# Kernel tuning notes

Hardware: AMD Instinct MI355X
Metric: run time of the kernel (lower is better)

Reference implementation:

```python
import jax, jax.numpy as jnp
import numpy as np
from jax.scipy.fft import dct

B, C, H, W = 64, 3, 512, 512


def dct2(x):
    # 2D DCT-II with ortho norm, matching scipy.fft.dct applied on axis=-1 then axis=-2
    x = dct(x, type=2, norm='ortho', axis=-1)
    x = dct(x, type=2, norm='ortho', axis=-2)
    return x


def setup_inputs() -> dict:
    key = jax.random.key(0)
    k1, k2, k3, k4 = jax.random.split(key, 4)
    return {
        'x': jax.random.normal(k1, (B, C, H, W), dtype=jnp.float32),
        'attention': jax.random.uniform(k2, (H, W), dtype=jnp.float32),
        'row_weights': jax.random.uniform(k3, (H,), dtype=jnp.float32),
        'col_weights': jax.random.uniform(k4, (W,), dtype=jnp.float32),
    }


def reference(x, attention, row_weights, col_weights):
    xd = dct2(x)                       # [B, C, H, W]
    gray = xd.mean(axis=1)             # [B, H, W] (channel mean)
    weighted = gray * attention        # [B, H, W]
    row_sum = weighted.mean(axis=2)    # [B, H] mean over W
    col_sum = weighted.mean(axis=1)    # [B, W] mean over H
    row_out = (row_sum * row_weights).mean(axis=1)  # [B]
    col_out = (col_sum * col_weights).mean(axis=1)  # [B]
    return jax.nn.sigmoid(jnp.stack([col_out, row_out], axis=1))  # [B, 2]
```

## Files before the change

kernel.cpp:

```cpp
#include <hip/hip_runtime.h>
#include <math.h>

#define NN 512
#define MM (NN * NN)
#define HW (NN * NN)
#define CH 3

__device__ __forceinline__ float dct_s(int k) {
    return (k == 0) ? 0.04419417382415922f : 0.0625f;
}

__global__ void __launch_bounds__(256) k_stageA(
    const float* __restrict__ att, const float* __restrict__ rw,
    const float* __restrict__ cw, float* __restrict__ Tr, float* __restrict__ Tc)
{
    __shared__ float sD[2048];
    __shared__ float sRw[512];
    __shared__ float sAcc[256 * 9];
    const int tid = threadIdx.x;
    const int bx  = blockIdx.x;
    const int h0  = (bx >> 3) * 4;
    const int wp0 = (bx & 7) * 64;
    const int kc  = tid >> 6;
    const int wl  = tid & 63;
    const int wp  = wp0 + wl;
    const int hp0 = kc * 128;

    #pragma unroll
    for (int e = 0; e < 8; ++e) {
        int idx = tid * 8 + e;
        int hp = idx >> 2, i = idx & 3;
        int m = ((2 * (h0 + i) + 1) * hp) & 2047;
        sD[idx] = dct_s(hp) * cospif((float)m * (1.0f / 1024.0f));
    }
    sRw[tid] = rw[tid];
    sRw[256 + tid] = rw[256 + tid];
    __syncthreads();

    float ar0=0.f,ar1=0.f,ar2=0.f,ar3=0.f, as0=0.f,as1=0.f,as2=0.f,as3=0.f;
    #pragma unroll 4
    for (int t = 0; t < 128; ++t) {
        int hp = hp0 + t;
        float a = att[hp * NN + wp];
        float r = sRw[hp];
        float4 d = *reinterpret_cast<const float4*>(&sD[hp * 4]);
        float ra = r * a;
        ar0 += d.x * ra; as0 += d.x * a;
        ar1 += d.y * ra; as1 += d.y * a;
        ar2 += d.z * ra; as2 += d.z * a;
        ar3 += d.w * ra; as3 += d.w * a;
    }
    float* sa = &sAcc[tid * 9];
    sa[0]=ar0; sa[1]=ar1; sa[2]=ar2; sa[3]=ar3;
    sa[4]=as0; sa[5]=as1; sa[6]=as2; sa[7]=as3;
    __syncthreads();
    if (tid < 64) {
        float v[8];
        #pragma unroll
        for (int j = 0; j < 8; ++j)
            v[j] = sAcc[(0*64 + tid)*9 + j] + sAcc[(1*64 + tid)*9 + j]
                 + sAcc[(2*64 + tid)*9 + j] + sAcc[(3*64 + tid)*9 + j];
        float c = cw[wp0 + tid];
        #pragma unroll
        for (int i = 0; i < 4; ++i) {
            Tr[(h0 + i) * NN + wp0 + tid] = v[i];
            Tc[(h0 + i) * NN + wp0 + tid] = v[4 + i] * c;
        }
    }
}

__global__ void __launch_bounds__(256) k_stageB(
    const float* __restrict__ Tr, const float* __restrict__ Tc,
    float* __restrict__ Gr, float* __restrict__ Gc)
{
    __shared__ float sT[512 * 8];
    __shared__ float sAcc[256 * 9];
    const int tid = threadIdx.x;
    const int bx  = blockIdx.x;
    const int h0  = (bx >> 3) * 4;
    const int w0  = (bx & 7) * 64;
    const int kc  = tid >> 6;
    const int wl  = tid & 63;
    const int w   = w0 + wl;
    const int wp0 = kc * 128;

    #pragma unroll
    for (int i = 0; i < 4; ++i) {
        sT[tid * 8 + i]             = Tr[(h0 + i) * NN + tid];
        sT[tid * 8 + 4 + i]         = Tc[(h0 + i) * NN + tid];
        sT[(tid + 256) * 8 + i]     = Tr[(h0 + i) * NN + tid + 256];
        sT[(tid + 256) * 8 + 4 + i] = Tc[(h0 + i) * NN + tid + 256];
    }
    __syncthreads();

    float gr0=0.f,gr1=0.f,gr2=0.f,gr3=0.f, gc0=0.f,gc1=0.f,gc2=0.f,gc3=0.f;
    const int w2 = 2 * w + 1;
    int m = (w2 * wp0) & 2047;
    #pragma unroll 4
    for (int t = 0; t < 128; ++t) {
        int wp = wp0 + t;
        float s = (wp == 0) ? 0.04419417382415922f : 0.0625f;
        float d = s * cospif((float)m * (1.0f / 1024.0f));
        m = (m + w2) & 2047;
        float4 ta = *reinterpret_cast<const float4*>(&sT[wp * 8]);
        float4 tb = *reinterpret_cast<const float4*>(&sT[wp * 8 + 4]);
        gr0 += ta.x * d; gr1 += ta.y * d; gr2 += ta.z * d; gr3 += ta.w * d;
        gc0 += tb.x * d; gc1 += tb.y * d; gc2 += tb.z * d; gc3 += tb.w * d;
    }
    float* sa = &sAcc[tid * 9];
    sa[0]=gr0; sa[1]=gr1; sa[2]=gr2; sa[3]=gr3;
    sa[4]=gc0; sa[5]=gc1; sa[6]=gc2; sa[7]=gc3;
    __syncthreads();
    if (tid < 64) {
        float v[8];
        #pragma unroll
        for (int j = 0; j < 8; ++j)
            v[j] = sAcc[(0*64 + tid)*9 + j] + sAcc[(1*64 + tid)*9 + j]
                 + sAcc[(2*64 + tid)*9 + j] + sAcc[(3*64 + tid)*9 + j];
        #pragma unroll
        for (int i = 0; i < 4; ++i) {
            Gr[(h0 + i) * NN + w0 + tid] = v[i];
            Gc[(h0 + i) * NN + w0 + tid] = v[4 + i];
        }
    }
}

__global__ void __launch_bounds__(256) k_reduce(
    const float* __restrict__ x, const float* __restrict__ Gr,
    const float* __restrict__ Gc, float* __restrict__ partials)
{
    const int b = blockIdx.y, ck = blockIdx.x, t = threadIdx.x;
    const float* xb = x + (size_t)b * (CH * HW);
    const int hw0 = ck * (HW / 32);
    float accr = 0.f, accc = 0.f;
    #pragma unroll 4
    for (int j = 0; j < 8; ++j) {
        int hw = hw0 + j * 1024 + t * 4;
        float4 gr = *(const float4*)(Gr + hw);
        float4 gc = *(const float4*)(Gc + hw);
        float4 x0 = *(const float4*)(xb + hw);
        float4 x1 = *(const float4*)(xb + HW + hw);
        float4 x2 = *(const float4*)(xb + 2 * HW + hw);
        float sxx = x0.x + x1.x + x2.x;
        float sxy = x0.y + x1.y + x2.y;
        float sxz = x0.z + x1.z + x2.z;
        float sxw = x0.w + x1.w + x2.w;
        accr += gr.x * sxx + gr.y * sxy + gr.z * sxz + gr.w * sxw;
        accc += gc.x * sxx + gc.y * sxy + gc.z * sxz + gc.w * sxw;
    }
    for (int off = 32; off > 0; off >>= 1) {
        accr += __shfl_down(accr, off);
        accc += __shfl_down(accc, off);
    }
    __shared__ float sr[4], sc[4];
    int wid = t >> 6;
    if ((t & 63) == 0) { sr[wid] = accr; sc[wid] = accc; }
    __syncthreads();
    if (t == 0) {
        partials[(b * 32 + ck) * 2 + 0] = sr[0] + sr[1] + sr[2] + sr[3];
        partials[(b * 32 + ck) * 2 + 1] = sc[0] + sc[1] + sc[2] + sc[3];
    }
}

__global__ void k_final(const float* __restrict__ partials, float* __restrict__ out) {
    int b = threadIdx.x;
    float r = 0.f, c = 0.f;
    for (int i = 0; i < 32; ++i) {
        r += partials[(b * 32 + i) * 2 + 0];
        c += partials[(b * 32 + i) * 2 + 1];
    }
    const float inv = 1.0f / (float)(CH * HW);
    r *= inv; c *= inv;
    out[b * 2 + 0] = 1.0f / (1.0f + expf(-c));
    out[b * 2 + 1] = 1.0f / (1.0f + expf(-r));
}

extern "C" void kernel_launch(void* const* d_in, const int* in_sizes, int n_in,
                              void* d_out, int out_size, void* d_ws, size_t ws_size,
                              hipStream_t stream) {
    const float* x   = (const float*)d_in[0];
    const float* att = (const float*)d_in[1];
    const float* rw  = (const float*)d_in[2];
    const float* cw  = (const float*)d_in[3];
    float* out = (float*)d_out;

    float* ws = (float*)d_ws;
    float* Tr = ws;
    float* Tc = ws + 1 * MM;
    float* Gr = ws + 2 * MM;
    float* Gc = ws + 3 * MM;
    float* partials = ws + 4 * MM;

    k_stageA<<<1024, 256, 0, stream>>>(att, rw, cw, Tr, Tc);
    k_stageB<<<1024, 256, 0, stream>>>(Tr, Tc, Gr, Gc);
    dim3 g(32, 64);
    k_reduce<<<g, 256, 0, stream>>>(x, Gr, Gc, partials);
    k_final<<<1, 64, 0, stream>>>(partials, out);
}
```

Before: 84.62 us.

## Fuse final reduction into reduce kernel via atomic counter, process two batches per block

Merges the separate final-sum kernel into the reduce kernel using a global atomic counter, so the last block to finish computes the sigmoid outputs. Each reduce block now handles two batches, which halves the grid and reuses each Gr/Gc load across both batches. The change removes one kernel launch and cuts Gr/Gc traffic, at the cost of an atomic, thread fences, and fewer blocks in flight for the memory-bound read of x.

```diff
diff --git a/kernel.cpp b/kernel.cpp
--- a/kernel.cpp
+++ b/kernel.cpp
@@ -12,13 +12,15 @@
 
 __global__ void __launch_bounds__(256) k_stageA(
     const float* __restrict__ att, const float* __restrict__ rw,
-    const float* __restrict__ cw, float* __restrict__ Tr, float* __restrict__ Tc)
+    const float* __restrict__ cw, float* __restrict__ Tr, float* __restrict__ Tc,
+    unsigned int* __restrict__ counter)
 {
     __shared__ float sD[2048];
     __shared__ float sRw[512];
     __shared__ float sAcc[256 * 9];
     const int tid = threadIdx.x;
     const int bx  = blockIdx.x;
+    if (bx == 0 && tid == 0) *counter = 0u;
     const int h0  = (bx >> 3) * 4;
     const int wp0 = (bx & 7) * 64;
     const int kc  = tid >> 6;
@@ -125,54 +127,83 @@
     }
 }
 
-__global__ void __launch_bounds__(256) k_reduce(
+__global__ void __launch_bounds__(256) k_reduce_final(
     const float* __restrict__ x, const float* __restrict__ Gr,
-    const float* __restrict__ Gc, float* __restrict__ partials)
+    const float* __restrict__ Gc, float* __restrict__ partials,
+    unsigned int* __restrict__ counter, float* __restrict__ out)
 {
-    const int b = blockIdx.y, ck = blockIdx.x, t = threadIdx.x;
-    const float* xb = x + (size_t)b * (CH * HW);
+    const int ck = blockIdx.x;
+    const int b1 = blockIdx.y;
+    const int b2 = b1 + 32;
+    const int t  = threadIdx.x;
+    const float* xb1 = x + (size_t)b1 * (CH * HW);
+    const float* xb2 = x + (size_t)b2 * (CH * HW);
     const int hw0 = ck * (HW / 32);
-    float accr = 0.f, accc = 0.f;
-    #pragma unroll 4
+
+    float ar1 = 0.f, ac1 = 0.f, ar2 = 0.f, ac2 = 0.f;
+    #pragma unroll 2
     for (int j = 0; j < 8; ++j) {
         int hw = hw0 + j * 1024 + t * 4;
         float4 gr = *(const float4*)(Gr + hw);
         float4 gc = *(const float4*)(Gc + hw);
-        float4 x0 = *(const float4*)(xb + hw);
-        float4 x1 = *(const float4*)(xb + HW + hw);
-        float4 x2 = *(const float4*)(xb + 2 * HW + hw);
-        float sxx = x0.x + x1.x + x2.x;
-        float sxy = x0.y + x1.y + x2.y;
-        float sxz = x0.z + x1.z + x2.z;
-        float sxw = x0.w + x1.w + x2.w;
-        accr += gr.x * sxx + gr.y * sxy + gr.z * sxz + gr.w * sxw;
-        accc += gc.x * sxx + gc.y * sxy + gc.z * sxz + gc.w * sxw;
+        float4 p0 = *(const float4*)(xb1 + hw);
+        float4 p1 = *(const float4*)(xb1 + HW + hw);
+        float4 p2 = *(const float4*)(xb1 + 2 * HW + hw);
+        float4 q0 = *(const float4*)(xb2 + hw);
+        float4 q1 = *(const float4*)(xb2 + HW + hw);
+        float4 q2 = *(const float4*)(xb2 + 2 * HW + hw);
+        float s1x = p0.x + p1.x + p2.x, s1y = p0.y + p1.y + p2.y;
+        float s1z = p0.z + p1.z + p2.z, s1w = p0.w + p1.w + p2.w;
+        float s2x = q0.x + q1.x + q2.x, s2y = q0.y + q1.y + q2.y;
+        float s2z = q0.z + q1.z + q2.z, s2w = q0.w + q1.w + q2.w;
+        ar1 += gr.x * s1x + gr.y * s1y + gr.z * s1z + gr.w * s1w;
+        ac1 += gc.x * s1x + gc.y * s1y + gc.z * s1z + gc.w * s1w;
+        ar2 += gr.x * s2x + gr.y * s2y + gr.z * s2z + gr.w * s2w;
+        ac2 += gc.x * s2x + gc.y * s2y + gc.z * s2z + gc.w * s2w;
     }
     for (int off = 32; off > 0; off >>= 1) {
-        accr += __shfl_down(accr, off);
-        accc += __shfl_down(accc, off);
-    }
-    __shared__ float sr[4], sc[4];
+        ar1 += __shfl_down(ar1, off);
+        ac1 += __shfl_down(ac1, off);
+        ar2 += __shfl_down(ar2, off);
+        ac2 += __shfl_down(ac2, off);
+    }
+    __shared__ float sm[4][4];
+    __shared__ bool sdone;
     int wid = t >> 6;
-    if ((t & 63) == 0) { sr[wid] = accr; sc[wid] = accc; }
+    if ((t & 63) == 0) {
+        sm[wid][0] = ar1; sm[wid][1] = ac1; sm[wid][2] = ar2; sm[wid][3] = ac2;
+    }
     __syncthreads();
     if (t == 0) {
-        partials[(b * 32 + ck) * 2 + 0] = sr[0] + sr[1] + sr[2] + sr[3];
-        partials[(b * 32 + ck) * 2 + 1] = sc[0] + sc[1] + sc[2] + sc[3];
-    }
-}
-
-__global__ void k_final(const float* __restrict__ partials, float* __restrict__ out) {
-    int b = threadIdx.x;
-    float r = 0.f, c = 0.f;
-    for (int i = 0; i < 32; ++i) {
-        r += partials[(b * 32 + i) * 2 + 0];
-        c += partials[(b * 32 + i) * 2 + 1];
-    }
-    const float inv = 1.0f / (float)(CH * HW);
-    r *= inv; c *= inv;
-    out[b * 2 + 0] = 1.0f / (1.0f + expf(-c));
-    out[b * 2 + 1] = 1.0f / (1.0f + expf(-r));
+        float r1 = sm[0][0] + sm[1][0] + sm[2][0] + sm[3][0];
+        float c1 = sm[0][1] + sm[1][1] + sm[2][1] + sm[3][1];
+        float r2 = sm[0][2] + sm[1][2] + sm[2][2] + sm[3][2];
+        float c2 = sm[0][3] + sm[1][3] + sm[2][3] + sm[3][3];
+        partials[(b1 * 32 + ck) * 2 + 0] = r1;
+        partials[(b1 * 32 + ck) * 2 + 1] = c1;
+        partials[(b2 * 32 + ck) * 2 + 0] = r2;
+        partials[(b2 * 32 + ck) * 2 + 1] = c2;
+        __threadfence();
+        unsigned int old = atomicAdd(counter, 1u);
+        sdone = (old == 32u * 32u - 1u);
+    }
+    __syncthreads();
+    if (sdone) {
+        __threadfence();
+        if (t < 64) {
+            float r = 0.f, c = 0.f;
+            #pragma unroll
+            for (int i = 0; i < 32; ++i) {
+                r += partials[(t * 32 + i) * 2 + 0];
+                c += partials[(t * 32 + i) * 2 + 1];
+            }
+            const float inv = 1.0f / (float)(CH * HW);
+            r *= inv; c *= inv;
+            out[t * 2 + 0] = 1.0f / (1.0f + expf(-c));
+            out[t * 2 + 1] = 1.0f / (1.0f + expf(-r));
+        }
+        if (t == 0) *counter = 0u;
+    }
 }
 
 extern "C" void kernel_launch(void* const* d_in, const int* in_sizes, int n_in,
@@ -190,10 +221,10 @@
     float* Gr = ws + 2 * MM;
     float* Gc = ws + 3 * MM;
     float* partials = ws + 4 * MM;
-
-    k_stageA<<<1024, 256, 0, stream>>>(att, rw, cw, Tr, Tc);
+    unsigned int* counter = (unsigned int*)(ws + 4 * MM + 4096);
+
+    k_stageA<<<1024, 256, 0, stream>>>(att, rw, cw, Tr, Tc, counter);
     k_stageB<<<1024, 256, 0, stream>>>(Tr, Tc, Gr, Gc);
-    dim3 g(32, 64);
-    k_reduce<<<g, 256, 0, stream>>>(x, Gr, Gc, partials);
-    k_final<<<1, 64, 0, stream>>>(partials, out);
-}
+    dim3 g(32, 32);
+    k_reduce_final<<<g, 256, 0, stream>>>(x, Gr, Gc, partials, counter, out);
+}
```

Result: slower. 115.2 us (+36.1%).
